# Kernel optimization log

Measured on AMD Instinct MI355X. Metric: run time of the kernel, lower is better.

Reference implementation:

```python
import jax, jax.numpy as jnp
import numpy as np

B, N, ND, D, K = 2, 5000, 3, 128, 6

def _lin_init(key, fan_in, fan_out):
    # torch nn.Linear default: U(-1/sqrt(fan_in), 1/sqrt(fan_in)) for W and b
    k1, k2 = jax.random.split(key)
    bound = 1.0 / np.sqrt(fan_in)
    W = jax.random.uniform(k1, (fan_in, fan_out), minval=-bound, maxval=bound, dtype=jnp.float32)
    b = jax.random.uniform(k2, (fan_out,), minval=-bound, maxval=bound, dtype=jnp.float32)
    return W, b

def setup_inputs() -> dict:
    key = jax.random.key(0)
    ks = jax.random.split(key, 7)
    loc = jax.random.uniform(ks[0], (B, N, 2), dtype=jnp.float32)
    deadline = jax.random.uniform(ks[1], (B, N), dtype=jnp.float32)
    depot = jax.random.uniform(ks[2], (B, 2), dtype=jnp.float32)
    W_init, b_init = _lin_init(ks[3], ND, D)      # init_embed: 3 -> 128
    W_nbr, b_nbr = _lin_init(ks[4], ND, D)        # neighbour_encode: 3 -> 128
    W_depot, b_depot = _lin_init(ks[5], 2, D)     # init_embed_depot: 2 -> 128
    W_final, b_final = _lin_init(ks[6], D, D)     # final_embedding: 128 -> 128
    return {"loc": loc, "deadline": deadline, "depot": depot,
            "W_init": W_init, "b_init": b_init,
            "W_nbr": W_nbr, "b_nbr": b_nbr,
            "W_depot": W_depot, "b_depot": b_depot,
            "W_final": W_final, "b_final": b_final}

def reference(loc, deadline, depot, W_init, b_init, W_nbr, b_nbr, W_depot, b_depot, W_final, b_final):
    x = jnp.concatenate([loc, deadline[:, :, None]], axis=2)          # [B,N,3]
    x2 = x[:, :, 0:2]                                                 # [B,N,2]
    F0 = x @ W_init + b_init                                          # [B,N,D]
    # pairwise L2 distances [B,N,N]
    dist = jnp.linalg.norm(x2[:, None, :, :] - x2[:, :, None, :], axis=-1)
    neighbors = jnp.argsort(dist, axis=-1)[:, :, :K]                  # [B,N,K]
    # faithful to torch `x[:, neighbors][0]`: gather features from batch 0
    neighbour = x[0][neighbors]                                       # [B,N,K,3]
    neighbour_delta = neighbour - x[:, :, None, :]                    # [B,N,K,3]
    nd_emb = neighbour_delta @ W_nbr + b_nbr                          # [B,N,K,D]
    concat = jnp.concatenate([F0[:, :, None, :], nd_emb], axis=2)     # [B,N,K+1,D]
    F_final = (concat @ W_final + b_final).sum(axis=2)                # [B,N,D]
    depot_emb = (depot @ W_depot + b_depot)[:, None, :]               # [B,1,D]
    h = jnp.concatenate([depot_emb, F_final], axis=1)                 # [B,N+1,D]
    return h, h.mean(axis=1)
```

## Files before the change

kernel.cpp:

```cpp
#include <hip/hip_runtime.h>
#include <hip/hip_bf16.h>

#define NB 2
#define NPTS 5000
#define DIM 128
#define G 64
#define NCELL (G*G)
#define HCELL (1.0f/G)
#define MEAN_OFF (2*5001*128)

#define WS_INT_F 41024
#define OFF_CSTART 0
#define OFF_CURSOR (NB*(NCELL+1))
#define OFF_PTSJ   (OFF_CURSOR + NB*NCELL)
#define N_INTS     (OFF_PTSJ + NB*NPTS)
#define WS_XY_F    (WS_INT_F + N_INTS)

__global__ __launch_bounds__(256) void pre_kernel(
    const float* __restrict__ W_init, const float* __restrict__ b_init,
    const float* __restrict__ W_nbr,  const float* __restrict__ b_nbr,
    const float* __restrict__ W_depot,const float* __restrict__ b_depot,
    const float* __restrict__ W_final,const float* __restrict__ b_final,
    const float* __restrict__ depot,
    float* __restrict__ ws, float* __restrict__ out) {
  const int tid = threadIdx.x;
  const int blk = blockIdx.x;
  if (blk < 3) {
    int idx = blk*256 + tid;
    const float* Ws = (idx < 384) ? W_init : W_nbr;
    int rem = (idx >= 384) ? idx - 384 : idx;
    int t = rem >> 7, d = rem & 127;
    float a0=0.f, a1=0.f, a2=0.f, a3=0.f;
#pragma unroll 8
    for (int e = 0; e < 128; e += 4) {
      a0 += Ws[t*128 + e]   * W_final[(e)*128 + d];
      a1 += Ws[t*128 + e+1] * W_final[(e+1)*128 + d];
      a2 += Ws[t*128 + e+2] * W_final[(e+2)*128 + d];
      a3 += Ws[t*128 + e+3] * W_final[(e+3)*128 + d];
    }
    ws[idx] = (a0+a1)+(a2+a3);
    return;
  }
  int* __restrict__ cz = (int*)(ws + WS_INT_F) + OFF_CURSOR;
  for (int idx = tid; idx < NB*NCELL; idx += 256) cz[idx] = 0;
  if (tid < 128) {
    float a0=0.f, a1=0.f, a2=0.f, a3=0.f;
#pragma unroll 8
    for (int e = 0; e < 128; e += 4) {
      a0 += (b_init[e]   + 6.f*b_nbr[e])   * W_final[(e)*128 + tid];
      a1 += (b_init[e+1] + 6.f*b_nbr[e+1]) * W_final[(e+1)*128 + tid];
      a2 += (b_init[e+2] + 6.f*b_nbr[e+2]) * W_final[(e+2)*128 + tid];
      a3 += (b_init[e+3] + 6.f*b_nbr[e+3]) * W_final[(e+3)*128 + tid];
    }
    ws[768 + tid] = (a0+a1)+(a2+a3) + 7.f*b_final[tid];
  }
  {
    int b = tid >> 7, d = tid & 127;
    float val = depot[b*2] * W_depot[d] + depot[b*2+1] * W_depot[128 + d] + b_depot[d];
    out[(size_t)b*5001*128 + d] = val;
    out[MEAN_OFF + b*128 + d]   = val * (1.f/5001.f);
  }
}

__device__ __forceinline__ int cell_of(float v) {
  int c = (int)(v * (float)G);
  return c < 0 ? 0 : (c > G-1 ? G-1 : c);
}

__global__ __launch_bounds__(256) void count_kernel(
    const float* __restrict__ loc, int* __restrict__ ints) {
  int tid = blockIdx.x*256 + threadIdx.x;
  if (tid >= NB*NPTS) return;
  int b = tid >= NPTS;
  float2 p = ((const float2*)loc)[tid];
  int c = cell_of(p.y)*G + cell_of(p.x);
  atomicAdd(&ints[OFF_CURSOR + b*NCELL + c], 1);
}

__global__ __launch_bounds__(1024) void scan_kernel(int* __restrict__ ints) {
  const int b = blockIdx.x, t = threadIdx.x;
  __shared__ int part[1024];
  int* cnt = ints + OFF_CURSOR + b*NCELL;
  int* cst = ints + OFF_CSTART + b*(NCELL+1);
  int c0 = cnt[4*t], c1 = cnt[4*t+1], c2 = cnt[4*t+2], c3 = cnt[4*t+3];
  int tot = c0+c1+c2+c3;
  part[t] = tot;
  __syncthreads();
  for (int off = 1; off < 1024; off <<= 1) {
    int v = (t >= off) ? part[t-off] : 0;
    __syncthreads();
    part[t] += v;
    __syncthreads();
  }
  int base = part[t] - tot;
  cst[4*t]   = base;            cnt[4*t]   = base;
  cst[4*t+1] = base+c0;         cnt[4*t+1] = base+c0;
  cst[4*t+2] = base+c0+c1;      cnt[4*t+2] = base+c0+c1;
  cst[4*t+3] = base+c0+c1+c2;   cnt[4*t+3] = base+c0+c1+c2;
  if (t == 1023) cst[NCELL] = part[1023];
}

__global__ __launch_bounds__(256) void scatter_kernel(
    const float* __restrict__ loc, int* __restrict__ ints,
    float2* __restrict__ xy) {
  int tid = blockIdx.x*256 + threadIdx.x;
  if (tid >= NB*NPTS) return;
  int b = tid >= NPTS;
  int i = tid - b*NPTS;
  float2 p = ((const float2*)loc)[tid];
  int c = cell_of(p.y)*G + cell_of(p.x);
  int pos = atomicAdd(&ints[OFF_CURSOR + b*NCELL + c], 1);
  xy[b*NPTS + pos] = p;
  ints[OFF_PTSJ + b*NPTS + pos] = i;
}

#define PACK(d_, j_) ((((unsigned long long)__float_as_uint(d_)) << 32) | (unsigned)(j_))
#define KINIT 0x7f800000ffffffffULL
#define INS6(nk) \
  { bool c_; unsigned long long t_; \
    c_ = nk<k0; t_=k0; k0=c_?nk:k0; nk=c_?t_:nk; \
    c_ = nk<k1; t_=k1; k1=c_?nk:k1; nk=c_?t_:nk; \
    c_ = nk<k2; t_=k2; k2=c_?nk:k2; nk=c_?t_:nk; \
    c_ = nk<k3; t_=k3; k3=c_?nk:k3; nk=c_?t_:nk; \
    c_ = nk<k4; t_=k4; k4=c_?nk:k4; nk=c_?t_:nk; \
    c_ = nk<k5; k5=c_?nk:k5; }

#define SCAN_RANGE(p0_, p1_) \
  for (int p = (p0_); p < (p1_); ++p) { \
    float2 t = sxy[p]; \
    float dx = q.x - t.x, dy = q.y - t.y; \
    float ss = __fadd_rn(__fmul_rn(dx,dx), __fmul_rn(dy,dy)); \
    float nd = sqrtf(ss); \
    unsigned long long nk = PACK(nd, (unsigned)sj[p]); \
    if (nk < k5) { INS6(nk); } }

__global__ __launch_bounds__(256) void knn_grid(
    const float* __restrict__ loc, const float* __restrict__ deadline,
    const int* __restrict__ ints, const float2* __restrict__ xy,
    float* __restrict__ nbrsum) {
  const int b = blockIdx.y;
  __shared__ float2 sxy[NPTS];
  __shared__ int    sj[NPTS];
  const float2* XY = xy + b*NPTS;
  const int*    J  = ints + OFF_PTSJ + b*NPTS;
  for (int k = threadIdx.x; k < NPTS; k += 256) { sxy[k] = XY[k]; sj[k] = J[k]; }
  __syncthreads();

  const int s = blockIdx.x*256 + threadIdx.x;
  if (s >= NPTS) return;
  const int* __restrict__ cs = ints + OFF_CSTART + b*(NCELL+1);

  const float2 q = sxy[s];
  const int qi = sj[s];
  const int cx = cell_of(q.x), cy = cell_of(q.y);
  const int x0 = cx-2 < 0 ? 0 : cx-2, x1 = cx+2 > G-1 ? G-1 : cx+2;

  unsigned long long k0=KINIT,k1=KINIT,k2=KINIT,k3=KINIT,k4=KINIT,k5=KINIT;

  int rb0,re0,rb1,re1,rb2,re2,rb3,re3,rb4,re4;
  {
    int y;
    y = cy-2; if (y >= 0 && y <= G-1) { rb0 = cs[y*G+x0]; re0 = cs[y*G+x1+1]; } else { rb0 = 0; re0 = 0; }
    y = cy-1; if (y >= 0 && y <= G-1) { rb1 = cs[y*G+x0]; re1 = cs[y*G+x1+1]; } else { rb1 = 0; re1 = 0; }
    y = cy;                           { rb2 = cs[y*G+x0]; re2 = cs[y*G+x1+1]; }
    y = cy+1; if (y >= 0 && y <= G-1) { rb3 = cs[y*G+x0]; re3 = cs[y*G+x1+1]; } else { rb3 = 0; re3 = 0; }
    y = cy+2; if (y >= 0 && y <= G-1) { rb4 = cs[y*G+x0]; re4 = cs[y*G+x1+1]; } else { rb4 = 0; re4 = 0; }
  }
  SCAN_RANGE(rb0, re0);
  SCAN_RANGE(rb1, re1);
  SCAN_RANGE(rb2, re2);
  SCAN_RANGE(rb3, re3);
  SCAN_RANGE(rb4, re4);

  int Rb = 2;
  while (true) {
    float d6 = __uint_as_float((unsigned)(k5 >> 32));
    if (0.999999f * ((float)Rb * HCELL) > d6) break;
    ++Rb;
    if (Rb > G) break;
    int xa = cx-Rb < 0 ? 0 : cx-Rb, xb = cx+Rb > G-1 ? G-1 : cx+Rb;
    int yt = cy-Rb, yb = cy+Rb;
    if (yt >= 0)   { int p0 = cs[yt*G+xa], p1 = cs[yt*G+xb+1]; SCAN_RANGE(p0, p1); }
    if (yb <= G-1) { int p0 = cs[yb*G+xa], p1 = cs[yb*G+xb+1]; SCAN_RANGE(p0, p1); }
    int ya = cy-Rb+1 < 0 ? 0 : cy-Rb+1, yz = cy+Rb-1 > G-1 ? G-1 : cy+Rb-1;
    if (cx-Rb >= 0)   { for (int y = ya; y <= yz; ++y) { int p0 = cs[y*G+(cx-Rb)], p1 = cs[y*G+(cx-Rb)+1]; SCAN_RANGE(p0, p1); } }
    if (cx+Rb <= G-1) { for (int y = ya; y <= yz; ++y) { int p0 = cs[y*G+(cx+Rb)], p1 = cs[y*G+(cx+Rb)+1]; SCAN_RANGE(p0, p1); } }
  }

  float s0=0.f, s1=0.f, s2=0.f;
  { int j=(int)(unsigned)k0; s0+=loc[j*2]; s1+=loc[j*2+1]; s2+=deadline[j]; }
  { int j=(int)(unsigned)k1; s0+=loc[j*2]; s1+=loc[j*2+1]; s2+=deadline[j]; }
  { int j=(int)(unsigned)k2; s0+=loc[j*2]; s1+=loc[j*2+1]; s2+=deadline[j]; }
  { int j=(int)(unsigned)k3; s0+=loc[j*2]; s1+=loc[j*2+1]; s2+=deadline[j]; }
  { int j=(int)(unsigned)k4; s0+=loc[j*2]; s1+=loc[j*2+1]; s2+=deadline[j]; }
  { int j=(int)(unsigned)k5; s0+=loc[j*2]; s1+=loc[j*2+1]; s2+=deadline[j]; }
  const size_t o = ((size_t)b*NPTS + qi) * 4;
  nbrsum[o] = s0; nbrsum[o+1] = s1; nbrsum[o+2] = s2;
}

__global__ __launch_bounds__(256) void rows_kernel(
    const float* __restrict__ loc, const float* __restrict__ deadline,
    const float* __restrict__ ws, float* __restrict__ out) {
  const int b  = blockIdx.y;
  const int d  = threadIdx.x & 127;
  const int rs = threadIdx.x >> 7;
  const float A0 = ws[d],      A1 = ws[128+d], A2 = ws[256+d];
  const float B0 = ws[384+d],  B1 = ws[512+d], B2 = ws[640+d];
  const float cc = ws[768+d];
  const float* __restrict__ nbrsum = ws + 1024;
  float msum = 0.f;
#pragma unroll
  for (int it = 0; it < 8; ++it) {
    int i = blockIdx.x*16 + it*2 + rs;
    if (i < NPTS) {
      size_t r = (size_t)b*NPTS + i;
      float u0 = loc[r*2], u1 = loc[r*2+1], u2 = deadline[r];
      float w0 = nbrsum[r*4]   - 6.f*u0;
      float w1 = nbrsum[r*4+1] - 6.f*u1;
      float w2 = nbrsum[r*4+2] - 6.f*u2;
      float val = cc + u0*A0 + u1*A1 + u2*A2 + w0*B0 + w1*B1 + w2*B2;
      out[((size_t)b*5001 + 1 + i)*128 + d] = val;
      msum += val;
    }
  }
  atomicAdd(&out[MEAN_OFF + b*128 + d], msum * (1.f/5001.f));
}

extern "C" void kernel_launch(void* const* d_in, const int* in_sizes, int n_in,
                              void* d_out, int out_size, void* d_ws, size_t ws_size,
                              hipStream_t stream) {
  const float* loc      = (const float*)d_in[0];
  const float* deadline = (const float*)d_in[1];
  const float* depot    = (const float*)d_in[2];
  const float* W_init   = (const float*)d_in[3];
  const float* b_init   = (const float*)d_in[4];
  const float* W_nbr    = (const float*)d_in[5];
  const float* b_nbr    = (const float*)d_in[6];
  const float* W_depot  = (const float*)d_in[7];
  const float* b_depot  = (const float*)d_in[8];
  const float* W_final  = (const float*)d_in[9];
  const float* b_final  = (const float*)d_in[10];
  float* out = (float*)d_out;
  float* ws  = (float*)d_ws;
  int*    ints = (int*)(ws + WS_INT_F);
  float2* xy   = (float2*)(ws + WS_XY_F);

  hipLaunchKernelGGL(pre_kernel, dim3(4), dim3(256), 0, stream,
                     W_init, b_init, W_nbr, b_nbr, W_depot, b_depot,
                     W_final, b_final, depot, ws, out);
  hipLaunchKernelGGL(count_kernel, dim3((NB*NPTS + 255)/256), dim3(256), 0, stream,
                     loc, ints);
  hipLaunchKernelGGL(scan_kernel, dim3(NB), dim3(1024), 0, stream, ints);
  hipLaunchKernelGGL(scatter_kernel, dim3((NB*NPTS + 255)/256), dim3(256), 0, stream,
                     loc, ints, xy);
  hipLaunchKernelGGL(knn_grid, dim3((NPTS + 255)/256, NB), dim3(256), 0, stream,
                     loc, deadline, ints, xy, ws + 1024);
  hipLaunchKernelGGL(rows_kernel, dim3((NPTS + 15)/16, NB), dim3(256), 0, stream,
                     loc, deadline, ws, out);
}
```

Measured before the change: 133.9 us.

## Fuse grid count, scan and scatter into one single-block shared-memory setup kernel

Merges the weight precompute, cell histogram, prefix scan and scatter into one launch. The bucketing runs in a single 1024-thread block per pass using a shared-memory histogram, which replaces global atomics and the separate zeroing of the cursor array. This cuts the launch count from six to three and removes global round trips between the grid-building stages. The cost is that the bucketing for both batches runs serially on one block, and the order of points within a cell still depends on shared atomics.

Measured after the change: 137.0 us. +2.3%, slower.

```diff
diff --git a/kernel.cpp b/kernel.cpp
--- a/kernel.cpp
+++ b/kernel.cpp
@@ -11,12 +11,17 @@
 
 #define WS_INT_F 41024
 #define OFF_CSTART 0
-#define OFF_CURSOR (NB*(NCELL+1))
-#define OFF_PTSJ   (OFF_CURSOR + NB*NCELL)
+#define OFF_PTSJ   (NB*(NCELL+1))
 #define N_INTS     (OFF_PTSJ + NB*NPTS)
-#define WS_XY_F    (WS_INT_F + N_INTS)
-
-__global__ __launch_bounds__(256) void pre_kernel(
+#define WS_XY_F    (WS_INT_F + N_INTS + 2)
+
+__device__ __forceinline__ int cell_of(float v) {
+  int c = (int)(v * (float)G);
+  return c < 0 ? 0 : (c > G-1 ? G-1 : c);
+}
+
+__global__ __launch_bounds__(1024) void setup_kernel(
+    const float* __restrict__ loc,
     const float* __restrict__ W_init, const float* __restrict__ b_init,
     const float* __restrict__ W_nbr,  const float* __restrict__ b_nbr,
     const float* __restrict__ W_depot,const float* __restrict__ b_depot,
@@ -26,92 +31,88 @@
   const int tid = threadIdx.x;
   const int blk = blockIdx.x;
   if (blk < 3) {
-    int idx = blk*256 + tid;
-    const float* Ws = (idx < 384) ? W_init : W_nbr;
-    int rem = (idx >= 384) ? idx - 384 : idx;
-    int t = rem >> 7, d = rem & 127;
-    float a0=0.f, a1=0.f, a2=0.f, a3=0.f;
+    if (tid < 256) {
+      int idx = blk*256 + tid;
+      const float* Ws = (idx < 384) ? W_init : W_nbr;
+      int rem = (idx >= 384) ? idx - 384 : idx;
+      int t = rem >> 7, d = rem & 127;
+      float a0=0.f, a1=0.f, a2=0.f, a3=0.f;
 #pragma unroll 8
-    for (int e = 0; e < 128; e += 4) {
-      a0 += Ws[t*128 + e]   * W_final[(e)*128 + d];
-      a1 += Ws[t*128 + e+1] * W_final[(e+1)*128 + d];
-      a2 += Ws[t*128 + e+2] * W_final[(e+2)*128 + d];
-      a3 += Ws[t*128 + e+3] * W_final[(e+3)*128 + d];
-    }
-    ws[idx] = (a0+a1)+(a2+a3);
+      for (int e = 0; e < 128; e += 4) {
+        a0 += Ws[t*128 + e]   * W_final[(e)*128 + d];
+        a1 += Ws[t*128 + e+1] * W_final[(e+1)*128 + d];
+        a2 += Ws[t*128 + e+2] * W_final[(e+2)*128 + d];
+        a3 += Ws[t*128 + e+3] * W_final[(e+3)*128 + d];
+      }
+      ws[idx] = (a0+a1)+(a2+a3);
+    }
     return;
   }
-  int* __restrict__ cz = (int*)(ws + WS_INT_F) + OFF_CURSOR;
-  for (int idx = tid; idx < NB*NCELL; idx += 256) cz[idx] = 0;
-  if (tid < 128) {
-    float a0=0.f, a1=0.f, a2=0.f, a3=0.f;
+  if (blk == 3) {
+    if (tid < 128) {
+      float a0=0.f, a1=0.f, a2=0.f, a3=0.f;
 #pragma unroll 8
-    for (int e = 0; e < 128; e += 4) {
-      a0 += (b_init[e]   + 6.f*b_nbr[e])   * W_final[(e)*128 + tid];
-      a1 += (b_init[e+1] + 6.f*b_nbr[e+1]) * W_final[(e+1)*128 + tid];
-      a2 += (b_init[e+2] + 6.f*b_nbr[e+2]) * W_final[(e+2)*128 + tid];
-      a3 += (b_init[e+3] + 6.f*b_nbr[e+3]) * W_final[(e+3)*128 + tid];
-    }
-    ws[768 + tid] = (a0+a1)+(a2+a3) + 7.f*b_final[tid];
-  }
-  {
-    int b = tid >> 7, d = tid & 127;
-    float val = depot[b*2] * W_depot[d] + depot[b*2+1] * W_depot[128 + d] + b_depot[d];
-    out[(size_t)b*5001*128 + d] = val;
-    out[MEAN_OFF + b*128 + d]   = val * (1.f/5001.f);
-  }
-}
-
-__device__ __forceinline__ int cell_of(float v) {
-  int c = (int)(v * (float)G);
-  return c < 0 ? 0 : (c > G-1 ? G-1 : c);
-}
-
-__global__ __launch_bounds__(256) void count_kernel(
-    const float* __restrict__ loc, int* __restrict__ ints) {
-  int tid = blockIdx.x*256 + threadIdx.x;
-  if (tid >= NB*NPTS) return;
-  int b = tid >= NPTS;
-  float2 p = ((const float2*)loc)[tid];
-  int c = cell_of(p.y)*G + cell_of(p.x);
-  atomicAdd(&ints[OFF_CURSOR + b*NCELL + c], 1);
-}
-
-__global__ __launch_bounds__(1024) void scan_kernel(int* __restrict__ ints) {
-  const int b = blockIdx.x, t = threadIdx.x;
+      for (int e = 0; e < 128; e += 4) {
+        a0 += (b_init[e]   + 6.f*b_nbr[e])   * W_final[(e)*128 + tid];
+        a1 += (b_init[e+1] + 6.f*b_nbr[e+1]) * W_final[(e+1)*128 + tid];
+        a2 += (b_init[e+2] + 6.f*b_nbr[e+2]) * W_final[(e+2)*128 + tid];
+        a3 += (b_init[e+3] + 6.f*b_nbr[e+3]) * W_final[(e+3)*128 + tid];
+      }
+      ws[768 + tid] = (a0+a1)+(a2+a3) + 7.f*b_final[tid];
+    }
+    if (tid < 256) {
+      int b = tid >> 7, d = tid & 127;
+      float val = depot[b*2] * W_depot[d] + depot[b*2+1] * W_depot[128 + d] + b_depot[d];
+      out[(size_t)b*5001*128 + d] = val;
+      out[MEAN_OFF + b*128 + d]   = val * (1.f/5001.f);
+    }
+    return;
+  }
+  __shared__ int hist[NCELL];
+  __shared__ int cellid[NPTS];
   __shared__ int part[1024];
-  int* cnt = ints + OFF_CURSOR + b*NCELL;
-  int* cst = ints + OFF_CSTART + b*(NCELL+1);
-  int c0 = cnt[4*t], c1 = cnt[4*t+1], c2 = cnt[4*t+2], c3 = cnt[4*t+3];
-  int tot = c0+c1+c2+c3;
-  part[t] = tot;
-  __syncthreads();
-  for (int off = 1; off < 1024; off <<= 1) {
-    int v = (t >= off) ? part[t-off] : 0;
-    __syncthreads();
-    part[t] += v;
-    __syncthreads();
-  }
-  int base = part[t] - tot;
-  cst[4*t]   = base;            cnt[4*t]   = base;
-  cst[4*t+1] = base+c0;         cnt[4*t+1] = base+c0;
-  cst[4*t+2] = base+c0+c1;      cnt[4*t+2] = base+c0+c1;
-  cst[4*t+3] = base+c0+c1+c2;   cnt[4*t+3] = base+c0+c1+c2;
-  if (t == 1023) cst[NCELL] = part[1023];
-}
-
-__global__ __launch_bounds__(256) void scatter_kernel(
-    const float* __restrict__ loc, int* __restrict__ ints,
-    float2* __restrict__ xy) {
-  int tid = blockIdx.x*256 + threadIdx.x;
-  if (tid >= NB*NPTS) return;
-  int b = tid >= NPTS;
-  int i = tid - b*NPTS;
-  float2 p = ((const float2*)loc)[tid];
-  int c = cell_of(p.y)*G + cell_of(p.x);
-  int pos = atomicAdd(&ints[OFF_CURSOR + b*NCELL + c], 1);
-  xy[b*NPTS + pos] = p;
-  ints[OFF_PTSJ + b*NPTS + pos] = i;
+  int* __restrict__ ints = (int*)(ws + WS_INT_F);
+  float2* __restrict__ xy = (float2*)(ws + WS_XY_F);
+  for (int b = 0; b < NB; ++b) {
+    for (int k = tid; k < NCELL; k += 1024) hist[k] = 0;
+    __syncthreads();
+    for (int k = tid; k < NPTS; k += 1024) {
+      float2 p = ((const float2*)loc)[b*NPTS + k];
+      int c = cell_of(p.y)*G + cell_of(p.x);
+      cellid[k] = c;
+      atomicAdd(&hist[c], 1);
+    }
+    __syncthreads();
+    int c0 = hist[4*tid], c1 = hist[4*tid+1], c2 = hist[4*tid+2], c3 = hist[4*tid+3];
+    int tot = c0+c1+c2+c3;
+    part[tid] = tot;
+    __syncthreads();
+    for (int off = 1; off < 1024; off <<= 1) {
+      int v = (tid >= off) ? part[tid-off] : 0;
+      __syncthreads();
+      part[tid] += v;
+      __syncthreads();
+    }
+    int base = part[tid] - tot;
+    int* cst = ints + OFF_CSTART + b*(NCELL+1);
+    cst[4*tid]   = base;
+    cst[4*tid+1] = base+c0;
+    cst[4*tid+2] = base+c0+c1;
+    cst[4*tid+3] = base+c0+c1+c2;
+    if (tid == 1023) cst[NCELL] = part[1023];
+    hist[4*tid]   = base;
+    hist[4*tid+1] = base+c0;
+    hist[4*tid+2] = base+c0+c1;
+    hist[4*tid+3] = base+c0+c1+c2;
+    __syncthreads();
+    for (int k = tid; k < NPTS; k += 1024) {
+      float2 p = ((const float2*)loc)[b*NPTS + k];
+      int pos = atomicAdd(&hist[cellid[k]], 1);
+      xy[b*NPTS + pos] = p;
+      ints[OFF_PTSJ + b*NPTS + pos] = k;
+    }
+    __syncthreads();
+  }
 }
 
 #define PACK(d_, j_) ((((unsigned long long)__float_as_uint(d_)) << 32) | (unsigned)(j_))
@@ -136,11 +137,12 @@
 
 __global__ __launch_bounds__(256) void knn_grid(
     const float* __restrict__ loc, const float* __restrict__ deadline,
-    const int* __restrict__ ints, const float2* __restrict__ xy,
-    float* __restrict__ nbrsum) {
+    const float* __restrict__ ws, float* __restrict__ nbrsum) {
   const int b = blockIdx.y;
   __shared__ float2 sxy[NPTS];
   __shared__ int    sj[NPTS];
+  const int* __restrict__ ints = (const int*)(ws + WS_INT_F);
+  const float2* __restrict__ xy = (const float2*)(ws + WS_XY_F);
   const float2* XY = xy + b*NPTS;
   const int*    J  = ints + OFF_PTSJ + b*NPTS;
   for (int k = threadIdx.x; k < NPTS; k += 256) { sxy[k] = XY[k]; sj[k] = J[k]; }
@@ -242,19 +244,12 @@
   const float* b_final  = (const float*)d_in[10];
   float* out = (float*)d_out;
   float* ws  = (float*)d_ws;
-  int*    ints = (int*)(ws + WS_INT_F);
-  float2* xy   = (float2*)(ws + WS_XY_F);
-
-  hipLaunchKernelGGL(pre_kernel, dim3(4), dim3(256), 0, stream,
-                     W_init, b_init, W_nbr, b_nbr, W_depot, b_depot,
+
+  hipLaunchKernelGGL(setup_kernel, dim3(5), dim3(1024), 0, stream,
+                     loc, W_init, b_init, W_nbr, b_nbr, W_depot, b_depot,
                      W_final, b_final, depot, ws, out);
-  hipLaunchKernelGGL(count_kernel, dim3((NB*NPTS + 255)/256), dim3(256), 0, stream,
-                     loc, ints);
-  hipLaunchKernelGGL(scan_kernel, dim3(NB), dim3(1024), 0, stream, ints);
-  hipLaunchKernelGGL(scatter_kernel, dim3((NB*NPTS + 255)/256), dim3(256), 0, stream,
-                     loc, ints, xy);
   hipLaunchKernelGGL(knn_grid, dim3((NPTS + 255)/256, NB), dim3(256), 0, stream,
-                     loc, deadline, ints, xy, ws + 1024);
+                     loc, deadline, ws, ws + 1024);
   hipLaunchKernelGGL(rows_kernel, dim3((NPTS + 15)/16, NB), dim3(256), 0, stream,
                      loc, deadline, ws, out);
 }
```
